# Kernel tuning notes

Measured on AMD Instinct MI355X. Metric: run time of the kernel, lower is better.

Reference implementation:

```python
import jax, jax.numpy as jnp
import numpy as np

IN_C, OUT_C, MAX_SIZE = 512, 256, 256
N = MAX_SIZE * MAX_SIZE  # 65536 nodes
E = MAX_SIZE * MAX_SIZE  # 65536 edges (before self loops)
NEG_SLOPE = 0.2


def setup_inputs() -> dict:
    key = jax.random.key(0)
    ks = jax.random.split(key, 12)
    s = 1.0 / np.sqrt(IN_C)
    so = 1.0 / np.sqrt(OUT_C)
    return {
        "x": jax.random.normal(ks[0], (N, IN_C), dtype=jnp.float32),
        "x_mask": jnp.ones((N,), dtype=bool),
        "edge_index": jax.random.randint(ks[1], (2, E), 0, N),
        "edge_mask": jnp.ones((E,), dtype=bool),
        "vaild_mask": jnp.ones((MAX_SIZE, MAX_SIZE), dtype=bool),
        # self-loop Linear
        "W_self": jax.random.uniform(ks[2], (IN_C, OUT_C), jnp.float32, -s, s),
        "b_self": jax.random.uniform(ks[3], (OUT_C,), jnp.float32, -s, s),
        # GATv2Conv params (heads=1)
        "W_l": jax.random.uniform(ks[4], (IN_C, OUT_C), jnp.float32, -s, s),
        "b_l": jnp.zeros((OUT_C,), jnp.float32),
        "W_r": jax.random.uniform(ks[5], (IN_C, OUT_C), jnp.float32, -s, s),
        "b_r": jnp.zeros((OUT_C,), jnp.float32),
        "att": jax.random.uniform(ks[6], (OUT_C,), jnp.float32, -so, so),
        "conv_bias": jnp.zeros((OUT_C,), jnp.float32),
        # sk classifier (out_channels -> 1)
        "W_cls": jax.random.uniform(ks[7], (OUT_C, 1), jnp.float32, -so, so),
        "b_cls": jax.random.uniform(ks[8], (1,), jnp.float32, -so, so),
    }


def _forward(x, edge_index, W_self, b_self, W_l, b_l, W_r, b_r, att,
             conv_bias, W_cls, b_cls):
    n = x.shape[0]
    # PyG GATv2Conv adds self-loops by default
    loops = jnp.arange(n, dtype=edge_index.dtype)
    src = jnp.concatenate([edge_index[0], loops])
    dst = jnp.concatenate([edge_index[1], loops])

    x_l = x @ W_l + b_l  # source-side transform (n, out)
    x_r = x @ W_r + b_r  # target-side transform (n, out)

    # per-edge GATv2 attention logits
    h = jax.nn.leaky_relu(x_l[src] + x_r[dst], NEG_SLOPE)  # (Etot, out)
    e = h @ att  # (Etot,)

    # segment softmax over incoming edges of each target node
    m = jnp.full((n,), -jnp.inf, dtype=e.dtype).at[dst].max(e)
    p = jnp.exp(e - m[dst])
    denom = jax.ops.segment_sum(p, dst, num_segments=n)
    alpha = p / denom[dst]

    x_neigh = jax.ops.segment_sum(alpha[:, None] * x_l[src], dst,
                                  num_segments=n) + conv_bias
    x_out = (x @ W_self + b_self) + x_neigh

    # sinkhorn-style row softmax channel (sk_channel=1, n1=n2=max_size)
    ms = MAX_SIZE
    sk = (x_out @ W_cls + b_cls).reshape(ms, ms)
    sk = jax.nn.softmax(sk, axis=-1)
    x_out = x_out + sk.reshape(-1, 1)
    # n1*n2 == max_size**2, so the padded output equals x_out
    return x_out


def reference(x, x_mask, edge_index, edge_mask, vaild_mask, W_self, b_self,
              W_l, b_l, W_r, b_r, att, conv_bias, W_cls, b_cls):
    # masks are all-True (fully valid case): x_valid = x, edges all kept
    return _forward(x, edge_index, W_self, b_self, W_l, b_l, W_r, b_r, att,
                    conv_bias, W_cls, b_cls)
```

## Files before the change

kernel.cpp:

```cpp
#include <hip/hip_runtime.h>
#include <hip/hip_bf16.h>
#include <stdint.h>

#define NNODE 65536
#define NEDGE 65536
#define ETOT  (NNODE + NEDGE)
#define INC   512
#define OUTC  256
#define NEG_SLOPE 0.2f
#define SLOTCAP 32

typedef __attribute__((ext_vector_type(8))) __bf16 bf16x8;
typedef __attribute__((ext_vector_type(4))) float f32x4;

__device__ __forceinline__ float b2f(unsigned short u) {
  return __uint_as_float(((unsigned int)u) << 16);
}
__device__ __forceinline__ unsigned short f2b(float f) {
  unsigned int u = __float_as_uint(f);
  u += 0x7fffu + ((u >> 16) & 1u);
  return (unsigned short)(u >> 16);
}
__device__ __forceinline__ unsigned int pk2(float lo, float hi) {
  return (unsigned int)f2b(lo) | ((unsigned int)f2b(hi) << 16);
}
__device__ __forceinline__ float lrelu(float v) {
  return v > 0.f ? v : NEG_SLOPE * v;
}

__global__ __launch_bounds__(256) void cvt_x_kernel(const float* __restrict__ x,
                                                    unsigned short* __restrict__ xb) {
  size_t i = ((size_t)blockIdx.x * 256 + threadIdx.x) * 4;
  float4 v = *(const float4*)(x + i);
  ushort4 o = { f2b(v.x), f2b(v.y), f2b(v.z), f2b(v.w) };
  *(ushort4*)(xb + i) = o;
}

__global__ __launch_bounds__(256) void prep_w_kernel(
    const float* __restrict__ Wl, const float* __restrict__ Wr, const float* __restrict__ Ws,
    const float* __restrict__ bl, const float* __restrict__ br, const float* __restrict__ bs,
    unsigned short* __restrict__ WT, float* __restrict__ bcat) {
  int i = blockIdx.x * 256 + threadIdx.x;
  if (i < 768 * 512) {
    int o = i >> 9, k = i & 511;
    float v;
    if (o < 256)      v = Wl[k * 256 + o];
    else if (o < 512) v = Wr[k * 256 + (o - 256)];
    else              v = Ws[k * 256 + (o - 512)];
    WT[i] = f2b(v);
  }
  if (i < 768) {
    bcat[i] = (i < 256) ? bl[i] : (i < 512 ? br[i - 256] : bs[i - 512]);
  }
}

__global__ __launch_bounds__(256) void gemm_kernel(
    const unsigned short* __restrict__ Xb,
    const unsigned short* __restrict__ WT,
    const float* __restrict__ bcat,
    unsigned short* __restrict__ xl,
    unsigned short* __restrict__ xr,
    float* __restrict__ outSelf) {
  __shared__ __align__(16) char smem[32768];
  unsigned short* sm = (unsigned short*)smem;

  const int wid = blockIdx.x;
  const int xcd = wid & 7;
  const int local = wid >> 3;
  const int by = local % 6;
  const int rowt = xcd * 64 + local / 6;
  const int rowBase = rowt * 128;
  const int colBase = by * 128;

  const int tid = threadIdx.x;
  const int lane = tid & 63;
  const int w = tid >> 6;
  const int wm = (w >> 1) * 64;
  const int wn = (w & 1) * 64;

  f32x4 acc[4][4] = {};

  auto stage = [&](int kk, int buf) {
#pragma unroll
    for (int c = 0; c < 2; ++c) {
      const int qb = w * 64 + c * 256;
      const int q = qb + lane;
      const int sl = (q & 3) ^ ((q >> 3) & 3);
      const unsigned short* gA = Xb + (size_t)(rowBase + (q >> 2)) * 512 + kk + sl * 8;
      __builtin_amdgcn_global_load_lds(
          (const __attribute__((address_space(1))) void*)gA,
          (__attribute__((address_space(3))) void*)(sm + buf * 8192 + qb * 8), 16, 0, 0);
      const unsigned short* gB = WT + (size_t)(colBase + (q >> 2)) * 512 + kk + sl * 8;
      __builtin_amdgcn_global_load_lds(
          (const __attribute__((address_space(1))) void*)gB,
          (__attribute__((address_space(3))) void*)(sm + buf * 8192 + 4096 + qb * 8), 16, 0, 0);
    }
  };

  stage(0, 0);
  __syncthreads();

  for (int t = 0; t < 16; ++t) {
    const int buf = t & 1;
    if (t + 1 < 16) stage((t + 1) * 32, buf ^ 1);

    const unsigned short* As = sm + buf * 8192;
    const unsigned short* Bs = As + 4096;
    bf16x8 a_frag[4], b_frag[4];
#pragma unroll
    for (int m = 0; m < 4; ++m) {
      const int rA = wm + m * 16 + (lane & 15);
      a_frag[m] = *(const bf16x8*)&As[rA * 32 + (((lane >> 4) ^ ((rA >> 1) & 3)) << 3)];
    }
#pragma unroll
    for (int n = 0; n < 4; ++n) {
      const int rB = wn + n * 16 + (lane & 15);
      b_frag[n] = *(const bf16x8*)&Bs[rB * 32 + (((lane >> 4) ^ ((rB >> 1) & 3)) << 3)];
    }
#pragma unroll
    for (int m = 0; m < 4; ++m)
#pragma unroll
      for (int n = 0; n < 4; ++n)
        acc[m][n] = __builtin_amdgcn_mfma_f32_16x16x32_bf16(a_frag[m], b_frag[n], acc[m][n], 0, 0, 0);

    __syncthreads();
  }

  const int colOff = (by & 1) * 128;
  if (by < 4) {
    unsigned short* dst = (by < 2) ? xl : xr;
    float* eps = (float*)smem + w * 1088;
    float biasn[4];
#pragma unroll
    for (int n = 0; n < 4; ++n) biasn[n] = bcat[colBase + wn + n * 16 + (lane & 15)];
#pragma unroll
    for (int m = 0; m < 4; ++m) {
      __syncthreads();
#pragma unroll
      for (int n = 0; n < 4; ++n)
#pragma unroll
        for (int j = 0; j < 4; ++j)
          eps[((lane >> 4) * 4 + j) * 68 + n * 16 + (lane & 15)] = acc[m][n][j] + biasn[n];
      __syncthreads();
#pragma unroll
      for (int it = 0; it < 2; ++it) {
        const int r16 = (lane >> 3) + it * 8;
        const int c8 = (lane & 7) * 8;
        const float* src = eps + r16 * 68 + c8;
        float4 v0 = *(const float4*)src;
        float4 v1 = *(const float4*)(src + 4);
        uint4 o;
        o.x = pk2(v0.x, v0.y);
        o.y = pk2(v0.z, v0.w);
        o.z = pk2(v1.x, v1.y);
        o.w = pk2(v1.z, v1.w);
        const int grow = rowBase + wm + m * 16 + r16;
        const int gcol = colOff + wn + c8;
        *(uint4*)(dst + (size_t)grow * 256 + gcol) = o;
      }
    }
  } else {
#pragma unroll
    for (int n = 0; n < 4; ++n) {
      const int col = colBase + wn + n * 16 + (lane & 15);
      const float bias = bcat[col];
#pragma unroll
      for (int m = 0; m < 4; ++m) {
#pragma unroll
        for (int j = 0; j < 4; ++j) {
          const int row = rowBase + wm + m * 16 + (lane >> 4) * 4 + j;
          outSelf[(size_t)row * 256 + (col - 512)] = acc[m][n][j] + bias;
        }
      }
    }
  }
}

__global__ __launch_bounds__(256) void edge_logit_kernel(
    const int* __restrict__ ei,
    const unsigned short* __restrict__ xl,
    const unsigned short* __restrict__ xr,
    const float* __restrict__ att,
    int* __restrict__ cnt,
    int* __restrict__ slot_src,
    float* __restrict__ slot_e) {
  const int j = blockIdx.x * 8 + (threadIdx.x >> 5);
  const int lane = threadIdx.x & 31;
  int src, dst;
  if (j < NEDGE) { src = ei[j]; dst = ei[NEDGE + j]; }
  else           { src = j - NEDGE; dst = src; }
  const int c = lane * 8;
  uint4 ul = *(const uint4*)(xl + (size_t)src * 256 + c);
  uint4 ur = *(const uint4*)(xr + (size_t)dst * 256 + c);
  float4 a0 = *(const float4*)(att + c);
  float4 a1 = *(const float4*)(att + c + 4);
  float s = lrelu(b2f((unsigned short)ul.x) + b2f((unsigned short)ur.x)) * a0.x
          + lrelu(b2f((unsigned short)(ul.x >> 16)) + b2f((unsigned short)(ur.x >> 16))) * a0.y
          + lrelu(b2f((unsigned short)ul.y) + b2f((unsigned short)ur.y)) * a0.z
          + lrelu(b2f((unsigned short)(ul.y >> 16)) + b2f((unsigned short)(ur.y >> 16))) * a0.w
          + lrelu(b2f((unsigned short)ul.z) + b2f((unsigned short)ur.z)) * a1.x
          + lrelu(b2f((unsigned short)(ul.z >> 16)) + b2f((unsigned short)(ur.z >> 16))) * a1.y
          + lrelu(b2f((unsigned short)ul.w) + b2f((unsigned short)ur.w)) * a1.z
          + lrelu(b2f((unsigned short)(ul.w >> 16)) + b2f((unsigned short)(ur.w >> 16))) * a1.w;
#pragma unroll
  for (int off = 16; off; off >>= 1) s += __shfl_xor(s, off);
  if (lane == 0) {
    const int pos = atomicAdd(&cnt[dst], 1);
    if (pos < SLOTCAP) {
      slot_src[dst * SLOTCAP + pos] = src;
      slot_e[dst * SLOTCAP + pos] = s;
    }
  }
}

__global__ __launch_bounds__(256) void node_kernel(
    const int* __restrict__ cnt,
    const int* __restrict__ slot_src, const float* __restrict__ slot_e,
    const unsigned short* __restrict__ xl,
    const float* __restrict__ conv_bias,
    float* __restrict__ out,
    const float* __restrict__ Wcls, const float* __restrict__ bcls,
    float* __restrict__ logits) {
  const int n = blockIdx.x * 4 + (threadIdx.x >> 6);
  const int lane = threadIdx.x & 63;
  const int base = n * SLOTCAP;
  const int deg = cnt[n];

  float m = -1e30f;
  for (int k = 0; k < deg; ++k) m = fmaxf(m, slot_e[base + k]);
  float denom = 0.f;
  for (int k = 0; k < deg; ++k) denom += __expf(slot_e[base + k] - m);
  const float inv = 1.f / denom;

  const int c = lane * 4;
  float4 accv = {0.f, 0.f, 0.f, 0.f};
  for (int k = 0; k < deg; ++k) {
    const float alpha = __expf(slot_e[base + k] - m) * inv;
    const int src = slot_src[base + k];
    ushort4 u = *(const ushort4*)(xl + (size_t)src * 256 + c);
    accv.x += alpha * b2f(u.x);
    accv.y += alpha * b2f(u.y);
    accv.z += alpha * b2f(u.z);
    accv.w += alpha * b2f(u.w);
  }
  const size_t o = (size_t)n * 256 + c;
  float4 cur = *(const float4*)(out + o);
  float4 cb = *(const float4*)(conv_bias + c);
  cur.x += accv.x + cb.x;
  cur.y += accv.y + cb.y;
  cur.z += accv.z + cb.z;
  cur.w += accv.w + cb.w;
  *(float4*)(out + o) = cur;

  float4 wc = *(const float4*)(Wcls + c);
  float part = cur.x * wc.x + cur.y * wc.y + cur.z * wc.z + cur.w * wc.w;
#pragma unroll
  for (int off = 32; off; off >>= 1) part += __shfl_xor(part, off, 64);
  if (lane == 0) logits[n] = part + bcls[0];
}

__global__ __launch_bounds__(256) void sk_kernel(const float* __restrict__ logits,
                                                 float* __restrict__ out) {
  __shared__ float sv[256];
  __shared__ float red[256];
  const int r = blockIdx.x;
  const int t = threadIdx.x;
  const float v = logits[r * 256 + t];
  red[t] = v;
  __syncthreads();
  for (int d = 128; d; d >>= 1) {
    if (t < d) red[t] = fmaxf(red[t], red[t + d]);
    __syncthreads();
  }
  const float mx = red[0];
  __syncthreads();
  const float p = __expf(v - mx);
  red[t] = p;
  __syncthreads();
  for (int d = 128; d; d >>= 1) {
    if (t < d) red[t] += red[t + d];
    __syncthreads();
  }
  const float sum = red[0];
  sv[t] = p / sum;
  __syncthreads();
  const size_t rowbase = (size_t)r * 256 * 256;
  for (int i = 0; i < 256; ++i) {
    out[rowbase + (size_t)i * 256 + t] += sv[i];
  }
}

extern "C" void kernel_launch(void* const* d_in, const int* in_sizes, int n_in,
                              void* d_out, int out_size, void* d_ws, size_t ws_size,
                              hipStream_t stream) {
  const float* x        = (const float*)d_in[0];
  const int*   ei       = (const int*)d_in[2];
  const float* W_self   = (const float*)d_in[5];
  const float* b_self   = (const float*)d_in[6];
  const float* W_l      = (const float*)d_in[7];
  const float* b_l      = (const float*)d_in[8];
  const float* W_r      = (const float*)d_in[9];
  const float* b_r      = (const float*)d_in[10];
  const float* att      = (const float*)d_in[11];
  const float* conv_bias= (const float*)d_in[12];
  const float* W_cls    = (const float*)d_in[13];
  const float* b_cls    = (const float*)d_in[14];
  float* out = (float*)d_out;

  char* ws = (char*)d_ws;
  size_t off = 0;
  auto alloc = [&](size_t bytes) {
    char* p = ws + off;
    off += (bytes + 255) & ~(size_t)255;
    return p;
  };
  unsigned short* xb   = (unsigned short*)alloc((size_t)NNODE * INC * 2);
  unsigned short* WT   = (unsigned short*)alloc((size_t)768 * 512 * 2);
  float*          bcat = (float*)alloc(768 * 4);
  unsigned short* xlb  = (unsigned short*)alloc((size_t)NNODE * OUTC * 2);
  unsigned short* xrb  = (unsigned short*)alloc((size_t)NNODE * OUTC * 2);
  int*            cnt  = (int*)alloc((size_t)NNODE * 4);
  float*          logits  = (float*)alloc((size_t)NNODE * 4);
  int*   slot_src = (int*)xb;
  float* slot_e   = (float*)(xb + (size_t)NNODE * SLOTCAP * 2);
  (void)ws_size; (void)in_sizes; (void)n_in; (void)out_size;

  hipMemsetAsync(cnt, 0, (size_t)NNODE * 4, stream);

  cvt_x_kernel<<<(NNODE * INC) / (256 * 4), 256, 0, stream>>>(x, xb);
  prep_w_kernel<<<(768 * 512 + 255) / 256, 256, 0, stream>>>(W_l, W_r, W_self, b_l, b_r, b_self, WT, bcat);
  gemm_kernel<<<3072, 256, 0, stream>>>(xb, WT, bcat, xlb, xrb, out);
  edge_logit_kernel<<<ETOT / 8, 256, 0, stream>>>(ei, xlb, xrb, att, cnt, slot_src, slot_e);
  node_kernel<<<NNODE / 4, 256, 0, stream>>>(cnt, slot_src, slot_e, xlb, conv_bias,
                                             out, W_cls, b_cls, logits);
  sk_kernel<<<256, 256, 0, stream>>>(logits, out);
}
```

Before: 229.5 us.

## Triple-buffer GEMM LDS pipeline with vmcnt waits and split sk_kernel rows

Changes the GEMM main loop from double to triple buffering in LDS. Loads run two K-steps ahead, and each step waits on a partial vmcnt instead of a full __syncthreads. Each compute phase raises wave priority around the MFMA block and is fenced with sched_barrier. Separately, sk_kernel now runs 4x as many blocks, each adding to a quarter of the rows, so the final broadcast-add has more parallelism. The cost is 48KB of LDS per block, which may lower occupancy, and each sk row softmax is recomputed by four blocks.

```diff
diff --git a/kernel.cpp b/kernel.cpp
--- a/kernel.cpp
+++ b/kernel.cpp
@@ -61,7 +61,7 @@
     unsigned short* __restrict__ xl,
     unsigned short* __restrict__ xr,
     float* __restrict__ outSelf) {
-  __shared__ __align__(16) char smem[32768];
+  __shared__ __align__(16) char smem[49152];
   unsigned short* sm = (unsigned short*)smem;
 
   const int wid = blockIdx.x;
@@ -97,34 +97,53 @@
     }
   };
 
+#define COMPUTE(bufidx) { \
+    const unsigned short* As = sm + (bufidx) * 8192; \
+    const unsigned short* Bs = As + 4096; \
+    bf16x8 a_frag[4], b_frag[4]; \
+    _Pragma("unroll") \
+    for (int m = 0; m < 4; ++m) { \
+      const int rA = wm + m * 16 + (lane & 15); \
+      a_frag[m] = *(const bf16x8*)&As[rA * 32 + (((lane >> 4) ^ ((rA >> 1) & 3)) << 3)]; \
+    } \
+    _Pragma("unroll") \
+    for (int n = 0; n < 4; ++n) { \
+      const int rB = wn + n * 16 + (lane & 15); \
+      b_frag[n] = *(const bf16x8*)&Bs[rB * 32 + (((lane >> 4) ^ ((rB >> 1) & 3)) << 3)]; \
+    } \
+    __builtin_amdgcn_s_setprio(1); \
+    _Pragma("unroll") \
+    for (int m = 0; m < 4; ++m) \
+      _Pragma("unroll") \
+      for (int n = 0; n < 4; ++n) \
+        acc[m][n] = __builtin_amdgcn_mfma_f32_16x16x32_bf16(a_frag[m], b_frag[n], acc[m][n], 0, 0, 0); \
+    __builtin_amdgcn_s_setprio(0); \
+  }
+
   stage(0, 0);
-  __syncthreads();
-
-  for (int t = 0; t < 16; ++t) {
-    const int buf = t & 1;
-    if (t + 1 < 16) stage((t + 1) * 32, buf ^ 1);
-
-    const unsigned short* As = sm + buf * 8192;
-    const unsigned short* Bs = As + 4096;
-    bf16x8 a_frag[4], b_frag[4];
-#pragma unroll
-    for (int m = 0; m < 4; ++m) {
-      const int rA = wm + m * 16 + (lane & 15);
-      a_frag[m] = *(const bf16x8*)&As[rA * 32 + (((lane >> 4) ^ ((rA >> 1) & 3)) << 3)];
-    }
-#pragma unroll
-    for (int n = 0; n < 4; ++n) {
-      const int rB = wn + n * 16 + (lane & 15);
-      b_frag[n] = *(const bf16x8*)&Bs[rB * 32 + (((lane >> 4) ^ ((rB >> 1) & 3)) << 3)];
-    }
-#pragma unroll
-    for (int m = 0; m < 4; ++m)
-#pragma unroll
-      for (int n = 0; n < 4; ++n)
-        acc[m][n] = __builtin_amdgcn_mfma_f32_16x16x32_bf16(a_frag[m], b_frag[n], acc[m][n], 0, 0, 0);
-
-    __syncthreads();
-  }
+  stage(32, 1);
+
+  for (int t = 0; t < 14; ++t) {
+    const int buf = t % 3;
+    stage((t + 2) * 32, (t + 2) % 3);
+    asm volatile("s_waitcnt vmcnt(8)" ::: "memory");
+    __builtin_amdgcn_s_barrier();
+    __builtin_amdgcn_sched_barrier(0);
+    COMPUTE(buf);
+    __builtin_amdgcn_sched_barrier(0);
+    __builtin_amdgcn_s_barrier();
+  }
+  asm volatile("s_waitcnt vmcnt(4)" ::: "memory");
+  __builtin_amdgcn_s_barrier();
+  __builtin_amdgcn_sched_barrier(0);
+  COMPUTE(2);
+  __builtin_amdgcn_sched_barrier(0);
+  __builtin_amdgcn_s_barrier();
+  asm volatile("s_waitcnt vmcnt(0)" ::: "memory");
+  __builtin_amdgcn_s_barrier();
+  __builtin_amdgcn_sched_barrier(0);
+  COMPUTE(0);
+#undef COMPUTE
 
   const int colOff = (by & 1) * 128;
   if (by < 4) {
@@ -263,7 +282,8 @@
                                                  float* __restrict__ out) {
   __shared__ float sv[256];
   __shared__ float red[256];
-  const int r = blockIdx.x;
+  const int r = blockIdx.x >> 2;
+  const int q = blockIdx.x & 3;
   const int t = threadIdx.x;
   const float v = logits[r * 256 + t];
   red[t] = v;
@@ -285,7 +305,7 @@
   sv[t] = p / sum;
   __syncthreads();
   const size_t rowbase = (size_t)r * 256 * 256;
-  for (int i = 0; i < 256; ++i) {
+  for (int i = q * 64; i < q * 64 + 64; ++i) {
     out[rowbase + (size_t)i * 256 + t] += sv[i];
   }
 }
@@ -333,5 +353,5 @@
   edge_logit_kernel<<<ETOT / 8, 256, 0, stream>>>(ei, xlb, xrb, att, cnt, slot_src, slot_e);
   node_kernel<<<NNODE / 4, 256, 0, stream>>>(cnt, slot_src, slot_e, xlb, conv_bias,
                                              out, W_cls, b_cls, logits);
-  sk_kernel<<<256, 256, 0, stream>>>(logits, out);
-}
+  sk_kernel<<<1024, 256, 0, stream>>>(logits, out);
+}
```

Measured after the change: 202.1 us. 1.14x faster.
